# Kernel tuning notes

Hardware: AMD Instinct MI355X
Metric: run time of the kernel (lower is better)

## Reference

```python
import jax, jax.numpy as jnp
import numpy as np

B, CIN, COUT, H, W = 4, 256, 256, 64, 64
KH, KW = 3, 3
STRIDE, PAD = 1, 1
K = KH * KW


def setup_inputs() -> dict:
    key = jax.random.key(0)
    k1, k2, k3 = jax.random.split(key, 3)
    x = jax.random.normal(k1, (B, CIN, H, W), dtype=jnp.float32)
    # small offset weights -> offsets of O(1) pixel, realistic near init
    offset_w = jax.random.normal(k2, (2 * K, CIN, KH, KW), dtype=jnp.float32) * 0.01
    offset_b = jnp.zeros((2 * K,), dtype=jnp.float32)
    dcn_w = jax.random.normal(k3, (COUT, CIN, KH, KW), dtype=jnp.float32) * (1.0 / np.sqrt(CIN * K))
    dcn_b = jnp.zeros((COUT,), dtype=jnp.float32)
    return {"x": x, "offset_w": offset_w, "offset_b": offset_b, "dcn_w": dcn_w, "dcn_b": dcn_b}


def _conv2d(x, w, b):
    y = jax.lax.conv_general_dilated(
        x, w, window_strides=(STRIDE, STRIDE),
        padding=((PAD, PAD), (PAD, PAD)),
        dimension_numbers=("NCHW", "OIHW", "NCHW"))
    return y + b[None, :, None, None]


def _bilinear_gather(x, py, px):
    """x: [B,C,H,W]; py,px: [B,K,Ho,Wo] float sample coords.
    Zero padding outside image (torchvision deform_conv2d semantics).
    Returns [B,C,K,Ho,Wo]."""
    Bb, C, Hin, Win = x.shape
    y0 = jnp.floor(py); x0 = jnp.floor(px)
    wy1 = py - y0; wx1 = px - x0
    y0i = y0.astype(jnp.int32); x0i = x0.astype(jnp.int32)
    x_flat = x.reshape(Bb, C, Hin * Win)

    def corner(yi, xi, wgt):
        valid = (yi >= 0) & (yi < Hin) & (xi >= 0) & (xi < Win)
        yc = jnp.clip(yi, 0, Hin - 1)
        xc = jnp.clip(xi, 0, Win - 1)
        idx = (yc * Win + xc).reshape(Bb, -1)  # [B, K*Ho*Wo]
        vals = jax.vmap(lambda xf, ix: jnp.take(xf, ix, axis=1))(x_flat, idx)
        vals = vals.reshape(Bb, C, *yi.shape[1:])  # [B,C,K,Ho,Wo]
        w_eff = jnp.where(valid, wgt, 0.0)[:, None]  # [B,1,K,Ho,Wo]
        return vals * w_eff

    out = corner(y0i, x0i, (1.0 - wy1) * (1.0 - wx1))
    out = out + corner(y0i, x0i + 1, (1.0 - wy1) * wx1)
    out = out + corner(y0i + 1, x0i, wy1 * (1.0 - wx1))
    out = out + corner(y0i + 1, x0i + 1, wy1 * wx1)
    return out


def _deformable_block(x, offset_w, offset_b, dcn_w, dcn_b):
    offset = _conv2d(x, offset_w, offset_b)  # [B, 2K, Ho, Wo]
    Bb, _, Ho, Wo = offset.shape
    off = offset.reshape(Bb, K, 2, Ho, Wo)
    dy, dx = off[:, :, 0], off[:, :, 1]  # torchvision: (y, x) interleaved per tap

    ky = jnp.repeat(jnp.arange(KH), KW).astype(jnp.float32)  # [K]
    kx = jnp.tile(jnp.arange(KW), KH).astype(jnp.float32)    # [K]
    base_y = (jnp.arange(Ho, dtype=jnp.float32) * STRIDE - PAD)[None, :, None] + ky[:, None, None]  # [K,Ho,1]
    base_x = (jnp.arange(Wo, dtype=jnp.float32) * STRIDE - PAD)[None, None, :] + kx[:, None, None]  # [K,1,Wo]
    py = base_y[None] + dy  # [B,K,Ho,Wo]
    px = base_x[None] + dx

    patches = _bilinear_gather(x, py, px)  # [B,C,K,Ho,Wo]
    wk = dcn_w.reshape(COUT, CIN, K)
    out = jnp.einsum("bckhw,ock->bohw", patches, wk)
    return out + dcn_b[None, :, None, None]


def reference(x, offset_w, offset_b, dcn_w, dcn_b):
    return _deformable_block(x, offset_w, offset_b, dcn_w, dcn_b)
```

## Files before the change

kernel.cpp:

```cpp
#include <hip/hip_runtime.h>

#define BB 4
#define CIN 256
#define COUT 256
#define HH 64
#define WW 64
#define KK 9
#define OC2 18
#define KTOT (CIN * KK)
#define NSTAGE 18

typedef __attribute__((ext_vector_type(8))) _Float16 h8;
typedef __attribute__((ext_vector_type(4))) float f32x4;

static __device__ __forceinline__ h8 splat_pk(unsigned pk) {
    union { unsigned u[4]; h8 h; } s;
    s.u[0] = pk; s.u[1] = pk; s.u[2] = pk; s.u[3] = pk;
    return s.h;
}

__global__ __launch_bounds__(256) void prework_kernel(
    const float* __restrict__ x, const float* __restrict__ ow,
    const float* __restrict__ dw,
    _Float16* __restrict__ xT, _Float16* __restrict__ bp,
    _Float16* __restrict__ bow)
{
    const int bid = blockIdx.x;
    const int t = threadIdx.x;
    if (bid < 1024) {
        const int b = bid >> 8, y = (bid >> 2) & 63, c0 = (bid & 3) * 64;
        __shared__ float tile[64][65];
#pragma unroll
        for (int r = 0; r < 16; ++r) {
            int idx = r * 256 + t;
            int c = idx >> 6, w = idx & 63;
            tile[c][w] = x[(((size_t)(b * CIN + c0 + c)) << 12) + (y << 6) + w];
        }
        __syncthreads();
        const int px = t >> 2;
#pragma unroll
        for (int half = 0; half < 2; ++half) {
            int cc = (t & 3) + half * 4;
            union { _Float16 h[8]; uint4 q; } u;
#pragma unroll
            for (int j = 0; j < 8; ++j) u.h[j] = (_Float16)tile[cc * 8 + j][px];
            size_t el = (((size_t)(b << 12)) + (y << 6) + px) * 256 + c0 + cc * 8;
            *(uint4*)&xT[el] = u.q;
        }
    } else if (bid < 1312) {
        int wid = (bid - 1024) * 256 + t;
        int T = wid >> 10;
        int r = wid & 1023;
        int cotile = r >> 6, lane = r & 63;
        int co = cotile * 16 + (lane & 15);
        int kbase = T * 32 + ((lane >> 4) & 3) * 8;
        union { _Float16 h[8]; uint4 q; } u;
#pragma unroll
        for (int j = 0; j < 8; ++j) {
            int k = kbase + j;
            int c = k & 255, kk = k >> 8;
            u.h[j] = (_Float16)dw[co * KTOT + c * KK + kk];
        }
        *(uint4*)&bp[(size_t)wid * 8] = u.q;
    } else {
        int wid = (bid - 1312) * 256 + t;
        int T = wid >> 7;
        int r = wid & 127;
        int lane = r & 63;
        int oc = ((r >> 6) << 4) + (lane & 15);
        int kbase = T * 32 + ((lane >> 4) & 3) * 8;
        union { _Float16 h[8]; uint4 q; } u;
#pragma unroll
        for (int j = 0; j < 8; ++j) {
            int k = kbase + j;
            int c = k & 255, kk = k >> 8;
            u.h[j] = (oc < OC2) ? (_Float16)ow[oc * KTOT + c * KK + kk] : (_Float16)0.f;
        }
        *(uint4*)&bow[(size_t)wid * 8] = u.q;
    }
}

__global__ __launch_bounds__(256) void offset_mfma_kernel(
    const _Float16* __restrict__ xT, const _Float16* __restrict__ bow,
    float* __restrict__ opart)
{
    const int bid = blockIdx.x;
    const int m_blk = bid >> 1, kh = bid & 1;
    const int b = m_blk >> 6;
    const int pxbase = (m_blk & 63) * 64;
    const int tid = threadIdx.x;
    const int lane = tid & 63, wv = tid >> 6;
    const int pin = lane & 15, kg = lane >> 4;

    __shared__ __align__(16) _Float16 Asl[2][2048];

    const _Float16* xb = xT + ((size_t)b << 20);
    const int pxl = pxbase + (wv << 4) + pin;
    const int py = pxl >> 6, px = pxl & 63;

    auto GLOAD = [&](int st, h8& R) {
        int kk = st >> 3;
        int ky = kk / 3, kx = kk - 3 * (kk / 3);
        int yy = py + ky - 1, xx = px + kx - 1;
        h8 v = {0, 0, 0, 0, 0, 0, 0, 0};
        if ((unsigned)yy < HH && (unsigned)xx < WW)
            v = *(const h8*)(xb + (((yy << 6) + xx) << 8) + (st & 7) * 32 + kg * 8);
        R = v;
    };
    auto BLOAD = [&](int st, uint4* br) {
#pragma unroll
        for (int nj = 0; nj < 2; ++nj)
            br[nj] = *(const uint4*)&bow[(size_t)(((st << 1) + nj) * 64 + lane) * 8];
    };

    f32x4 acc[2];
    {
        f32x4 z = {0.f, 0.f, 0.f, 0.f};
        acc[0] = z; acc[1] = z;
    }

    const int t0 = kh * 36;
    h8 RA, RB;
    uint4 bregA[2], bregB[2];

    GLOAD(t0, RA);
    GLOAD(t0 + 1, RB);
    BLOAD(t0, bregA);
    *(h8*)&Asl[0][tid * 8] = RA;
    __syncthreads();

    for (int tt = 0; tt < 36; tt += 2) {
        int st = t0 + tt;
        if (tt + 2 < 36) GLOAD(st + 2, RA);
        BLOAD(st + 1, bregB);
        {
            h8 a = *(const h8*)&Asl[0][tid * 8];
            union { uint4 q; h8 h; } bb;
#pragma unroll
            for (int nj = 0; nj < 2; ++nj) {
                bb.q = bregA[nj];
                acc[nj] = __builtin_amdgcn_mfma_f32_16x16x32_f16(a, bb.h, acc[nj], 0, 0, 0);
            }
        }
        *(h8*)&Asl[1][tid * 8] = RB;
        __syncthreads();
        if (tt + 3 < 36) GLOAD(st + 3, RB);
        if (tt + 2 < 36) BLOAD(st + 2, bregA);
        {
            h8 a = *(const h8*)&Asl[1][tid * 8];
            union { uint4 q; h8 h; } bb;
#pragma unroll
            for (int nj = 0; nj < 2; ++nj) {
                bb.q = bregB[nj];
                acc[nj] = __builtin_amdgcn_mfma_f32_16x16x32_f16(a, bb.h, acc[nj], 0, 0, 0);
            }
        }
        if (tt + 2 < 36) *(h8*)&Asl[0][tid * 8] = RA;
        __syncthreads();
    }

    const int pxb = pxbase + (wv << 4) + kg * 4;
#pragma unroll
    for (int nj = 0; nj < 2; ++nj) {
        int oc = nj * 16 + pin;
        if (oc < OC2) {
            float4 o;
            o.x = acc[nj][0]; o.y = acc[nj][1];
            o.z = acc[nj][2]; o.w = acc[nj][3];
            *(float4*)&opart[(((size_t)((kh * BB + b) * OC2 + oc)) << 12) + pxb] = o;
        }
    }
}

__global__ __launch_bounds__(512, 4) void dcn_mfma_kernel(
    const _Float16* __restrict__ xT, const float* __restrict__ opart,
    const float* __restrict__ ob, const _Float16* __restrict__ bp,
    const float* __restrict__ db, float* __restrict__ out)
{
    int P = blockIdx.x;
    int L = (P & 7) * 128 + (P >> 3);
    const int m_blk = L >> 1, n0 = L & 1;
    const int b = m_blk >> 7;
    const int rowbase = (m_blk & 127) * 32;

    const int tid = threadIdx.x;
    const int lane = tid & 63;
    const int wv = tid >> 6;
    const int kslice = lane >> 4, pxlo = lane & 15;

    const int g_px = tid >> 4;
    const int g_cg = tid & 15;
    const int g_ebase = g_px * 9;
    const int g_widx = (g_cg >> 2) * 128 + ((g_px >> 4) << 6) + (g_cg & 3) * 16
                     + ((g_px & 15) ^ (g_cg & 7));

    __shared__ __align__(16) _Float16 Asl[2][4096];
    __shared__ __align__(8) uint2 twA[288];
    __shared__ __align__(8) uint2 twB[288];
    __shared__ __align__(8) uint2 tih[288];

    const float* op0 = opart + (((size_t)(b * OC2)) << 12);
    const float* op1 = opart + (((size_t)((BB + b) * OC2)) << 12);
    if (tid < 288) {
        int e = tid;
        int p = e / 9, kk = e - (e / 9) * 9;
        int pxl = rowbase + p;
        int y = pxl >> 6, xx = pxl & 63;
        float dy = op0[((size_t)(2 * kk) << 12) + pxl]
                 + op1[((size_t)(2 * kk) << 12) + pxl] + ob[2 * kk];
        float dx = op0[((size_t)(2 * kk + 1) << 12) + pxl]
                 + op1[((size_t)(2 * kk + 1) << 12) + pxl] + ob[2 * kk + 1];
        int ky = kk / 3, kx = kk - 3 * (kk / 3);
        float sy = (float)(y - 1 + ky) + dy;
        float sx = (float)(xx - 1 + kx) + dx;
        float fy = floorf(sy), fx = floorf(sx);
        int y0 = (int)fy, x0 = (int)fx;
        float wy1 = sy - fy, wx1 = sx - fx;
        float wy0 = 1.f - wy1, wx0 = 1.f - wx1;
        bool vy0 = (unsigned)y0 < HH, vy1 = (unsigned)(y0 + 1) < HH;
        bool vx0 = (unsigned)x0 < WW, vx1 = (unsigned)(x0 + 1) < WW;
        _Float16 w00 = (_Float16)((vy0 && vx0) ? wy0 * wx0 : 0.f);
        _Float16 w01 = (_Float16)((vy0 && vx1) ? wy0 * wx1 : 0.f);
        _Float16 w10 = (_Float16)((vy1 && vx0) ? wy1 * wx0 : 0.f);
        _Float16 w11 = (_Float16)((vy1 && vx1) ? wy1 * wx1 : 0.f);
        union { _Float16 h[2]; unsigned u; } pk;
        uint2 WA, WB;
        pk.h[0] = w00; pk.h[1] = w00; WA.x = pk.u;
        pk.h[0] = w01; pk.h[1] = w01; WA.y = pk.u;
        pk.h[0] = w10; pk.h[1] = w10; WB.x = pk.u;
        pk.h[0] = w11; pk.h[1] = w11; WB.y = pk.u;
        twA[e] = WA;
        twB[e] = WB;
        int y0c = min(max(y0, 0), HH - 1), y1c = min(max(y0 + 1, 0), HH - 1);
        int x0c = min(max(x0, 0), WW - 1), x1c = min(max(x0 + 1, 0), WW - 1);
        unsigned i00 = (unsigned)((y0c << 6) + x0c);
        unsigned i01 = (unsigned)((y0c << 6) + x1c);
        unsigned i10 = (unsigned)((y1c << 6) + x0c);
        unsigned i11 = (unsigned)((y1c << 6) + x1c);
        tih[e] = make_uint2(i00 | (i01 << 16), i10 | (i11 << 16));
    }
    __syncthreads();

    const char* xbyte = (const char*)(xT + ((size_t)b << 20));

    auto GLOAD = [&](int st, h8& c00, h8& c01, h8& c10, h8& c11) {
        uint2 ij = tih[g_ebase + (st >> 1)];
        unsigned chb = (unsigned)((st & 1) * 256 + g_cg * 16);
        c00 = *(const h8*)(xbyte + (((ij.x & 0xFFFFu) << 9) + chb));
        c01 = *(const h8*)(xbyte + (((ij.x >> 16)     << 9) + chb));
        c10 = *(const h8*)(xbyte + (((ij.y & 0xFFFFu) << 9) + chb));
        c11 = *(const h8*)(xbyte + (((ij.y >> 16)     << 9) + chb));
    };
    auto GCONSUME = [&](int st, int buf, h8 c00, h8 c01, h8 c10, h8 c11) {
        int e = g_ebase + (st >> 1);
        uint2 wa = twA[e], wb = twB[e];
        h8 v = c00 * splat_pk(wa.x);
        v += c01 * splat_pk(wa.y);
        v += c10 * splat_pk(wb.x);
        v += c11 * splat_pk(wb.y);
        *(h8*)&Asl[buf][g_widx * 8] = v;
    };
    auto BLOAD = [&](int st, uint4* br) {
#pragma unroll
        for (int ks = 0; ks < 4; ++ks) {
            size_t word = ((size_t)((st * 4 + ks) * 16 + n0 * 8 + wv)) * 64 + lane;
            br[ks] = *(const uint4*)&bp[word * 8];
        }
    };

    f32x4 acc[2];
    {
        f32x4 z = {0.f, 0.f, 0.f, 0.f};
        acc[0] = z; acc[1] = z;
    }

    auto MFMA8 = [&](int buf, uint4* br) {
        __builtin_amdgcn_s_setprio(1);
#pragma unroll
        for (int ks = 0; ks < 4; ++ks) {
            int w0 = ks * 128 + kslice * 16 + (pxlo ^ ((ks * 4 + kslice) & 7));
            h8 a0 = *(const h8*)&Asl[buf][w0 * 8];
            h8 a1 = *(const h8*)&Asl[buf][(w0 + 64) * 8];
            union { uint4 q; h8 h; } bb; bb.q = br[ks];
            acc[0] = __builtin_amdgcn_mfma_f32_16x16x32_f16(a0, bb.h, acc[0], 0, 0, 0);
            acc[1] = __builtin_amdgcn_mfma_f32_16x16x32_f16(a1, bb.h, acc[1], 0, 0, 0);
        }
        __builtin_amdgcn_s_setprio(0);
    };

    h8 E0, E1, E2, E3, F0, F1, F2, F3;
    uint4 breg[4], bnext[4];

    GLOAD(0, E0, E1, E2, E3);
    GLOAD(1, F0, F1, F2, F3);
    BLOAD(0, breg);
    GCONSUME(0, 0, E0, E1, E2, E3);
    __syncthreads();

    for (int st = 0; st < NSTAGE; st += 2) {
        if (st + 2 < NSTAGE) GLOAD(st + 2, E0, E1, E2, E3);
        BLOAD(st + 1, bnext);
        MFMA8(0, breg);
        GCONSUME(st + 1, 1, F0, F1, F2, F3);
        __syncthreads();
        if (st + 3 < NSTAGE) GLOAD(st + 3, F0, F1, F2, F3);
        if (st + 2 < NSTAGE) BLOAD(st + 2, breg);
        MFMA8(1, bnext);
        if (st + 2 < NSTAGE) GCONSUME(st + 2, 0, E0, E1, E2, E3);
        __syncthreads();
    }

    const int co = n0 * 128 + wv * 16 + pxlo;
    const float bv = db[co];
    float* op = out + ((size_t)(b * COUT + co) << 12) + rowbase;
#pragma unroll
    for (int mi = 0; mi < 2; ++mi) {
        int pxoff = mi * 16 + kslice * 4;
        float4 o;
        o.x = acc[mi][0] + bv;
        o.y = acc[mi][1] + bv;
        o.z = acc[mi][2] + bv;
        o.w = acc[mi][3] + bv;
        *(float4*)&op[pxoff] = o;
    }
}

extern "C" void kernel_launch(void* const* d_in, const int* in_sizes, int n_in,
                              void* d_out, int out_size, void* d_ws, size_t ws_size,
                              hipStream_t stream)
{
    const float* x  = (const float*)d_in[0];
    const float* ow = (const float*)d_in[1];
    const float* ob = (const float*)d_in[2];
    const float* dw = (const float*)d_in[3];
    const float* db = (const float*)d_in[4];
    float* out = (float*)d_out;

    char* wsp = (char*)d_ws;
    float*     opart = (float*)wsp;
    _Float16*  bp    = (_Float16*)(wsp + 2359296);
    _Float16*  bow   = (_Float16*)(wsp + 3538944);
    _Float16*  xT    = (_Float16*)(wsp + 3686400);

    hipLaunchKernelGGL(prework_kernel,     dim3(1348), dim3(256), 0, stream, x, ow, dw, xT, bp, bow);
    hipLaunchKernelGGL(offset_mfma_kernel, dim3(512),  dim3(256), 0, stream, xT, bow, opart);
    hipLaunchKernelGGL(dcn_mfma_kernel,    dim3(1024), dim3(512), 0, stream, xT, opart, ob, bp, db, out);
}
```

Measured before the change: 77.09 us.

## Restructure deformable conv GEMM to full-N tiles with split-K waves and LDS-staged weights

The main DCN kernel now gives each block 64 pixels and all 256 output channels. Its eight waves form four M groups times two K halves, and the two halves are reduced through LDS at the end. The sampled A fragments stay in registers instead of going through LDS, and weight tiles are staged cooperatively into a 64KB double-buffered dynamic LDS region. The goal is to cut redundant bilinear gathers, which were done once per N half before, and to reuse B from LDS. The cost is 64 accumulator registers per lane, fewer blocks (256), and lower occupancy. The offset conv kernel also drops its LDS round-trip and uses bigger blocks.

```diff
diff --git a/kernel.cpp b/kernel.cpp
--- a/kernel.cpp
+++ b/kernel.cpp
@@ -8,7 +8,6 @@
 #define KK 9
 #define OC2 18
 #define KTOT (CIN * KK)
-#define NSTAGE 18
 
 typedef __attribute__((ext_vector_type(8))) _Float16 h8;
 typedef __attribute__((ext_vector_type(4))) float f32x4;
@@ -80,89 +79,69 @@
     }
 }
 
-__global__ __launch_bounds__(256) void offset_mfma_kernel(
+__global__ __launch_bounds__(512) void offset_mfma_kernel(
     const _Float16* __restrict__ xT, const _Float16* __restrict__ bow,
     float* __restrict__ opart)
 {
     const int bid = blockIdx.x;
     const int m_blk = bid >> 1, kh = bid & 1;
-    const int b = m_blk >> 6;
-    const int pxbase = (m_blk & 63) * 64;
+    const int b = m_blk >> 5;
+    const int pxbase = (m_blk & 31) * 128;
     const int tid = threadIdx.x;
     const int lane = tid & 63, wv = tid >> 6;
-    const int pin = lane & 15, kg = lane >> 4;
-
-    __shared__ __align__(16) _Float16 Asl[2][2048];
+    const int colg = lane & 15, kg = lane >> 4;
+
+    const int pxl = pxbase + (wv << 4) + colg;
+    const int py = pxl >> 6, pxx = pxl & 63;
 
     const _Float16* xb = xT + ((size_t)b << 20);
-    const int pxl = pxbase + (wv << 4) + pin;
-    const int py = pxl >> 6, px = pxl & 63;
-
-    auto GLOAD = [&](int st, h8& R) {
-        int kk = st >> 3;
+
+    auto GLOAD = [&](int T, h8& R) {
+        int kk = T >> 3;
         int ky = kk / 3, kx = kk - 3 * (kk / 3);
-        int yy = py + ky - 1, xx = px + kx - 1;
+        int yy = py + ky - 1, xx = pxx + kx - 1;
         h8 v = {0, 0, 0, 0, 0, 0, 0, 0};
         if ((unsigned)yy < HH && (unsigned)xx < WW)
-            v = *(const h8*)(xb + (((yy << 6) + xx) << 8) + (st & 7) * 32 + kg * 8);
+            v = *(const h8*)(xb + ((((yy << 6) + xx) << 8) + ((T & 7) << 5) + (kg << 3)));
         R = v;
     };
-    auto BLOAD = [&](int st, uint4* br) {
+    auto BLOAD = [&](int T, uint4* br) {
 #pragma unroll
         for (int nj = 0; nj < 2; ++nj)
-            br[nj] = *(const uint4*)&bow[(size_t)(((st << 1) + nj) * 64 + lane) * 8];
+            br[nj] = *(const uint4*)&bow[(size_t)(((T << 1) + nj) * 64 + lane) * 8];
     };
 
     f32x4 acc[2];
-    {
-        f32x4 z = {0.f, 0.f, 0.f, 0.f};
-        acc[0] = z; acc[1] = z;
-    }
-
-    const int t0 = kh * 36;
-    h8 RA, RB;
-    uint4 bregA[2], bregB[2];
-
-    GLOAD(t0, RA);
-    GLOAD(t0 + 1, RB);
-    BLOAD(t0, bregA);
-    *(h8*)&Asl[0][tid * 8] = RA;
-    __syncthreads();
-
-    for (int tt = 0; tt < 36; tt += 2) {
-        int st = t0 + tt;
-        if (tt + 2 < 36) GLOAD(st + 2, RA);
-        BLOAD(st + 1, bregB);
+    { f32x4 z = {0.f, 0.f, 0.f, 0.f}; acc[0] = z; acc[1] = z; }
+
+    const int Tb = kh * 36;
+    h8 E, F;
+    uint4 bA[2], bB[2];
+
+    GLOAD(Tb, E);
+    BLOAD(Tb, bA);
+    for (int r = 0; r < 36; r += 2) {
+        GLOAD(Tb + r + 1, F);
+        BLOAD(Tb + r + 1, bB);
         {
-            h8 a = *(const h8*)&Asl[0][tid * 8];
-            union { uint4 q; h8 h; } bb;
-#pragma unroll
-            for (int nj = 0; nj < 2; ++nj) {
-                bb.q = bregA[nj];
-                acc[nj] = __builtin_amdgcn_mfma_f32_16x16x32_f16(a, bb.h, acc[nj], 0, 0, 0);
-            }
-        }
-        *(h8*)&Asl[1][tid * 8] = RB;
-        __syncthreads();
-        if (tt + 3 < 36) GLOAD(st + 3, RB);
-        if (tt + 2 < 36) BLOAD(st + 2, bregA);
+            union { uint4 q; h8 h; } u0, u1;
+            u0.q = bA[0]; u1.q = bA[1];
+            acc[0] = __builtin_amdgcn_mfma_f32_16x16x32_f16(E, u0.h, acc[0], 0, 0, 0);
+            acc[1] = __builtin_amdgcn_mfma_f32_16x16x32_f16(E, u1.h, acc[1], 0, 0, 0);
+        }
+        if (r + 2 < 36) { GLOAD(Tb + r + 2, E); BLOAD(Tb + r + 2, bA); }
         {
-            h8 a = *(const h8*)&Asl[1][tid * 8];
-            union { uint4 q; h8 h; } bb;
-#pragma unroll
-            for (int nj = 0; nj < 2; ++nj) {
-                bb.q = bregB[nj];
-                acc[nj] = __builtin_amdgcn_mfma_f32_16x16x32_f16(a, bb.h, acc[nj], 0, 0, 0);
-            }
-        }
-        if (tt + 2 < 36) *(h8*)&Asl[0][tid * 8] = RA;
-        __syncthreads();
+            union { uint4 q; h8 h; } u0, u1;
+            u0.q = bB[0]; u1.q = bB[1];
+            acc[0] = __builtin_amdgcn_mfma_f32_16x16x32_f16(F, u0.h, acc[0], 0, 0, 0);
+            acc[1] = __builtin_amdgcn_mfma_f32_16x16x32_f16(F, u1.h, acc[1], 0, 0, 0);
+        }
     }
 
     const int pxb = pxbase + (wv << 4) + kg * 4;
 #pragma unroll
     for (int nj = 0; nj < 2; ++nj) {
-        int oc = nj * 16 + pin;
+        int oc = nj * 16 + colg;
         if (oc < OC2) {
             float4 o;
             o.x = acc[nj][0]; o.y = acc[nj][1];
@@ -172,37 +151,35 @@
     }
 }
 
-__global__ __launch_bounds__(512, 4) void dcn_mfma_kernel(
+__global__ __launch_bounds__(512, 2) void dcn_mfma_kernel(
     const _Float16* __restrict__ xT, const float* __restrict__ opart,
     const float* __restrict__ ob, const _Float16* __restrict__ bp,
     const float* __restrict__ db, float* __restrict__ out)
 {
+    extern __shared__ char smraw[];
+    _Float16* Bsl = (_Float16*)smraw;
+    uint2* twp = (uint2*)(smraw + 65536);
+    uint2* tih = (uint2*)(smraw + 65536 + 4608);
+
     int P = blockIdx.x;
-    int L = (P & 7) * 128 + (P >> 3);
-    const int m_blk = L >> 1, n0 = L & 1;
-    const int b = m_blk >> 7;
-    const int rowbase = (m_blk & 127) * 32;
+    int L = (P & 7) * 32 + (P >> 3);
+    const int b = L >> 6;
+    const int rowbase = (L & 63) * 64;
 
     const int tid = threadIdx.x;
     const int lane = tid & 63;
     const int wv = tid >> 6;
-    const int kslice = lane >> 4, pxlo = lane & 15;
-
-    const int g_px = tid >> 4;
-    const int g_cg = tid & 15;
-    const int g_ebase = g_px * 9;
-    const int g_widx = (g_cg >> 2) * 128 + ((g_px >> 4) << 6) + (g_cg & 3) * 16
-                     + ((g_px & 15) ^ (g_cg & 7));
-
-    __shared__ __align__(16) _Float16 Asl[2][4096];
-    __shared__ __align__(8) uint2 twA[288];
-    __shared__ __align__(8) uint2 twB[288];
-    __shared__ __align__(8) uint2 tih[288];
+    const int wm = wv & 3;
+    const int wk = wv >> 2;
+    const int colg = lane & 15;
+    const int kg = lane >> 4;
+
+    const int px_local = wm * 16 + colg;
+    const int ebase = px_local * 9;
 
     const float* op0 = opart + (((size_t)(b * OC2)) << 12);
     const float* op1 = opart + (((size_t)((BB + b) * OC2)) << 12);
-    if (tid < 288) {
-        int e = tid;
+    for (int e = tid; e < 576; e += 512) {
         int p = e / 9, kk = e - (e / 9) * 9;
         int pxl = rowbase + p;
         int y = pxl >> 6, xx = pxl & 63;
@@ -223,14 +200,11 @@
         _Float16 w01 = (_Float16)((vy0 && vx1) ? wy0 * wx1 : 0.f);
         _Float16 w10 = (_Float16)((vy1 && vx0) ? wy1 * wx0 : 0.f);
         _Float16 w11 = (_Float16)((vy1 && vx1) ? wy1 * wx1 : 0.f);
-        union { _Float16 h[2]; unsigned u; } pk;
-        uint2 WA, WB;
-        pk.h[0] = w00; pk.h[1] = w00; WA.x = pk.u;
-        pk.h[0] = w01; pk.h[1] = w01; WA.y = pk.u;
-        pk.h[0] = w10; pk.h[1] = w10; WB.x = pk.u;
-        pk.h[0] = w11; pk.h[1] = w11; WB.y = pk.u;
-        twA[e] = WA;
-        twB[e] = WB;
+        union { _Float16 h[2]; unsigned u; } pk2;
+        uint2 W;
+        pk2.h[0] = w00; pk2.h[1] = w01; W.x = pk2.u;
+        pk2.h[0] = w10; pk2.h[1] = w11; W.y = pk2.u;
+        twp[e] = W;
         int y0c = min(max(y0, 0), HH - 1), y1c = min(max(y0 + 1, 0), HH - 1);
         int x0c = min(max(x0, 0), WW - 1), x1c = min(max(x0 + 1, 0), WW - 1);
         unsigned i00 = (unsigned)((y0c << 6) + x0c);
@@ -243,85 +217,108 @@
 
     const char* xbyte = (const char*)(xT + ((size_t)b << 20));
 
-    auto GLOAD = [&](int st, h8& c00, h8& c01, h8& c10, h8& c11) {
-        uint2 ij = tih[g_ebase + (st >> 1)];
-        unsigned chb = (unsigned)((st & 1) * 256 + g_cg * 16);
-        c00 = *(const h8*)(xbyte + (((ij.x & 0xFFFFu) << 9) + chb));
-        c01 = *(const h8*)(xbyte + (((ij.x >> 16)     << 9) + chb));
-        c10 = *(const h8*)(xbyte + (((ij.y & 0xFFFFu) << 9) + chb));
-        c11 = *(const h8*)(xbyte + (((ij.y >> 16)     << 9) + chb));
-    };
-    auto GCONSUME = [&](int st, int buf, h8 c00, h8 c01, h8 c10, h8 c11) {
-        int e = g_ebase + (st >> 1);
-        uint2 wa = twA[e], wb = twB[e];
-        h8 v = c00 * splat_pk(wa.x);
-        v += c01 * splat_pk(wa.y);
-        v += c10 * splat_pk(wb.x);
-        v += c11 * splat_pk(wb.y);
-        *(h8*)&Asl[buf][g_widx * 8] = v;
-    };
-    auto BLOAD = [&](int st, uint4* br) {
-#pragma unroll
-        for (int ks = 0; ks < 4; ++ks) {
-            size_t word = ((size_t)((st * 4 + ks) * 16 + n0 * 8 + wv)) * 64 + lane;
-            br[ks] = *(const uint4*)&bp[word * 8];
-        }
-    };
-
-    f32x4 acc[2];
-    {
-        f32x4 z = {0.f, 0.f, 0.f, 0.f};
-        acc[0] = z; acc[1] = z;
-    }
-
-    auto MFMA8 = [&](int buf, uint4* br) {
+    auto AGLOAD = [&](int T, h8* C) {
+        uint2 ij = tih[ebase + (T >> 3)];
+        unsigned coff = (unsigned)(((T & 7) << 6) + (kg << 4));
+        C[0] = *(const h8*)(xbyte + (((ij.x & 0xFFFFu) << 9) + coff));
+        C[1] = *(const h8*)(xbyte + (((ij.x >> 16)     << 9) + coff));
+        C[2] = *(const h8*)(xbyte + (((ij.y & 0xFFFFu) << 9) + coff));
+        C[3] = *(const h8*)(xbyte + (((ij.y >> 16)     << 9) + coff));
+    };
+    auto COMBINE = [&](int T, const h8* C) -> h8 {
+        uint2 w = twp[ebase + (T >> 3)];
+        unsigned w00 = (w.x & 0xFFFFu) * 0x10001u;
+        unsigned w01 = (w.x >> 16)     * 0x10001u;
+        unsigned w10 = (w.y & 0xFFFFu) * 0x10001u;
+        unsigned w11 = (w.y >> 16)     * 0x10001u;
+        h8 v = C[0] * splat_pk(w00);
+        v += C[1] * splat_pk(w01);
+        v += C[2] * splat_pk(w10);
+        v += C[3] * splat_pk(w11);
+        return v;
+    };
+    auto BSTAGE_LOAD = [&](int r1, uint4* S) {
+#pragma unroll
+        for (int j = 0; j < 4; ++j) {
+            int s = tid + j * 512;
+            int kh2 = s >> 10;
+            int T = kh2 * 36 + r1;
+            size_t gw = (size_t)T * 1024 + (s & 1023);
+            S[j] = *(const uint4*)&bp[gw * 8];
+        }
+    };
+    auto BSTAGE_WRITE = [&](int bufp, const uint4* S) {
+#pragma unroll
+        for (int j = 0; j < 4; ++j) {
+            int s = tid + j * 512;
+            *(uint4*)&Bsl[((size_t)bufp * 2048 + s) * 8] = S[j];
+        }
+    };
+
+    f32x4 acc[16];
+#pragma unroll
+    for (int i = 0; i < 16; ++i) { f32x4 z = {0.f, 0.f, 0.f, 0.f}; acc[i] = z; }
+
+    auto MFMA16 = [&](int p, h8 v) {
+        const _Float16* base = &Bsl[(size_t)(p * 2 + wk) * 1024 * 8];
         __builtin_amdgcn_s_setprio(1);
 #pragma unroll
-        for (int ks = 0; ks < 4; ++ks) {
-            int w0 = ks * 128 + kslice * 16 + (pxlo ^ ((ks * 4 + kslice) & 7));
-            h8 a0 = *(const h8*)&Asl[buf][w0 * 8];
-            h8 a1 = *(const h8*)&Asl[buf][(w0 + 64) * 8];
-            union { uint4 q; h8 h; } bb; bb.q = br[ks];
-            acc[0] = __builtin_amdgcn_mfma_f32_16x16x32_f16(a0, bb.h, acc[0], 0, 0, 0);
-            acc[1] = __builtin_amdgcn_mfma_f32_16x16x32_f16(a1, bb.h, acc[1], 0, 0, 0);
+        for (int nj = 0; nj < 16; ++nj) {
+            union { uint4 q; h8 h; } bb;
+            bb.q = *(const uint4*)&base[(nj * 64 + lane) * 8];
+            acc[nj] = __builtin_amdgcn_mfma_f32_16x16x32_f16(v, bb.h, acc[nj], 0, 0, 0);
         }
         __builtin_amdgcn_s_setprio(0);
     };
 
-    h8 E0, E1, E2, E3, F0, F1, F2, F3;
-    uint4 breg[4], bnext[4];
-
-    GLOAD(0, E0, E1, E2, E3);
-    GLOAD(1, F0, F1, F2, F3);
-    BLOAD(0, breg);
-    GCONSUME(0, 0, E0, E1, E2, E3);
+    const int Tb = wk * 36;
+    h8 E[4], F[4];
+    uint4 S[4];
+
+    BSTAGE_LOAD(0, S);
+    AGLOAD(Tb, E);
+    BSTAGE_WRITE(0, S);
     __syncthreads();
 
-    for (int st = 0; st < NSTAGE; st += 2) {
-        if (st + 2 < NSTAGE) GLOAD(st + 2, E0, E1, E2, E3);
-        BLOAD(st + 1, bnext);
-        MFMA8(0, breg);
-        GCONSUME(st + 1, 1, F0, F1, F2, F3);
+    for (int r = 0; r < 36; r += 2) {
+        BSTAGE_LOAD(r + 1, S);
+        AGLOAD(Tb + r + 1, F);
+        {
+            h8 v = COMBINE(Tb + r, E);
+            MFMA16(0, v);
+        }
+        BSTAGE_WRITE(1, S);
         __syncthreads();
-        if (st + 3 < NSTAGE) GLOAD(st + 3, F0, F1, F2, F3);
-        if (st + 2 < NSTAGE) BLOAD(st + 2, breg);
-        MFMA8(1, bnext);
-        if (st + 2 < NSTAGE) GCONSUME(st + 2, 0, E0, E1, E2, E3);
+        if (r + 2 < 36) { BSTAGE_LOAD(r + 2, S); AGLOAD(Tb + r + 2, E); }
+        {
+            h8 v = COMBINE(Tb + r + 1, F);
+            MFMA16(1, v);
+        }
+        if (r + 2 < 36) BSTAGE_WRITE(0, S);
         __syncthreads();
     }
 
-    const int co = n0 * 128 + wv * 16 + pxlo;
-    const float bv = db[co];
-    float* op = out + ((size_t)(b * COUT + co) << 12) + rowbase;
-#pragma unroll
-    for (int mi = 0; mi < 2; ++mi) {
-        int pxoff = mi * 16 + kslice * 4;
-        float4 o;
-        o.x = acc[mi][0] + bv;
-        o.y = acc[mi][1] + bv;
-        o.z = acc[mi][2] + bv;
-        o.w = acc[mi][3] + bv;
-        *(float4*)&op[pxoff] = o;
+    f32x4* red = (f32x4*)smraw;
+    if (wk == 1) {
+#pragma unroll
+        for (int nj = 0; nj < 16; ++nj)
+            red[(wm * 16 + nj) * 64 + lane] = acc[nj];
+    }
+    __syncthreads();
+    if (wk == 0) {
+#pragma unroll
+        for (int nj = 0; nj < 16; ++nj) {
+            f32x4 o2 = red[(wm * 16 + nj) * 64 + lane];
+            int co = nj * 16 + colg;
+            float bv = db[co];
+            float* op = out + ((size_t)(b * COUT + co) << 12) + rowbase + wm * 16 + kg * 4;
+            float4 st;
+            st.x = acc[nj][0] + o2[0] + bv;
+            st.y = acc[nj][1] + o2[1] + bv;
+            st.z = acc[nj][2] + o2[2] + bv;
+            st.w = acc[nj][3] + o2[3] + bv;
+            *(float4*)op = st;
+        }
     }
 }
 
@@ -342,7 +339,13 @@
     _Float16*  bow   = (_Float16*)(wsp + 3538944);
     _Float16*  xT    = (_Float16*)(wsp + 3686400);
 
+    const int DYN_LDS = 65536 + 4608 + 4608;
+
+    hipFuncSetAttribute((const void*)dcn_mfma_kernel,
+                        hipFuncAttributeMaxDynamicSharedMemorySize, DYN_LDS);
+
     hipLaunchKernelGGL(prework_kernel,     dim3(1348), dim3(256), 0, stream, x, ow, dw, xT, bp, bow);
-    hipLaunchKernelGGL(offset_mfma_kernel, dim3(512),  dim3(256), 0, stream, xT, bow, opart);
-    hipLaunchKernelGGL(dcn_mfma_kernel,    dim3(1024), dim3(512), 0, stream, xT, opart, ob, bp, db, out);
-}
+    hipLaunchKernelGGL(offset_mfma_kernel, dim3(256),  dim3(512), 0, stream, xT, bow, opart);
+    hipLaunchKernelGGL(dcn_mfma_kernel,    dim3(256),  dim3(512), DYN_LDS, stream,
+                       xT, opart, ob, bp, db, out);
+}
```

New measurement: 133.2 us. +72.7%, slower.
